# Kernel tuning notes

Hardware: AMD Instinct MI355X
Metric: run time of the kernel (lower is better)

## Reference

```python
import jax, jax.numpy as jnp
import numpy as np

K, D, N, T, B = 8, 16, 32, 200, 2048
_LOG2PI = float(np.log(2.0 * np.pi))


def setup_inputs() -> dict:
    key = jax.random.key(0)
    ks = jax.random.split(key, 13)
    return {
        "discrete_states": jax.random.randint(ks[0], (B, T), 0, K),
        "continuous_states": jax.random.normal(ks[1], (B, T, D), dtype=jnp.float32),
        "obs": jax.random.normal(ks[2], (B, T, N), dtype=jnp.float32),
        "discrete_init_logits": jax.random.normal(ks[3], (K,), dtype=jnp.float32),
        "continuous_init_locs": jax.random.normal(ks[4], (K, D), dtype=jnp.float32),
        "continuous_init_log_scales": jax.random.normal(ks[5], (K, D), dtype=jnp.float32),
        "state_transition_logits": jax.random.normal(ks[6], (K, K), dtype=jnp.float32),
        "dynamics_matrices": jax.random.normal(ks[7], (K, D, D), dtype=jnp.float32) * 0.3,
        "dynamics_offsets": jax.random.normal(ks[8], (K, D), dtype=jnp.float32),
        # NOTE: original code uses dynamics_log_scales directly as a scale (missing .exp());
        # we keep that math faithfully but init it strictly positive to stay finite.
        "dynamics_log_scales": jax.random.uniform(ks[9], (K, D), minval=0.5, maxval=1.5, dtype=jnp.float32),
        "emission_matrices": jax.random.normal(ks[10], (K, N, D), dtype=jnp.float32),
        "emission_offsets": jax.random.normal(ks[11], (K, N), dtype=jnp.float32),
        "emission_log_scales": jax.random.normal(ks[12], (K, N), dtype=jnp.float32),
    }


def _normal_lp(x, loc, scale):
    # elementwise Normal log-prob
    return -0.5 * jnp.square((x - loc) / scale) - jnp.log(scale) - 0.5 * _LOG2PI


def reference(discrete_states, continuous_states, obs,
              discrete_init_logits, continuous_init_locs, continuous_init_log_scales,
              state_transition_logits, dynamics_matrices, dynamics_offsets,
              dynamics_log_scales, emission_matrices, emission_offsets,
              emission_log_scales):
    """log p(s_{1:T}, z_{1:T}, x_{1:T}) -> [B]"""
    s0 = discrete_states[:, 0]                      # [B]
    z0 = continuous_states[:, 0]                    # [B,D]
    # p(s_1)
    lp = jax.nn.log_softmax(discrete_init_logits)[s0]
    # p(z_1 | s_1)
    lp = lp + _normal_lp(z0, continuous_init_locs[s0],
                         jnp.exp(continuous_init_log_scales[s0])).sum(-1)
    # p(s_t | s_{t-1}) for t=2..T, fully vectorized over time
    s_prev = discrete_states[:, :-1]
    s_cur = discrete_states[:, 1:]
    trans = jax.nn.log_softmax(state_transition_logits, axis=-1)  # [K,K]
    lp = lp + trans[s_prev, s_cur].sum(-1)
    # p(z_t | z_{t-1}, s_t)
    A = dynamics_matrices[s_cur]                    # [B,T-1,D,D] gather
    dyn_loc = jnp.einsum('btij,btj->bti', A, continuous_states[:, :-1]) + dynamics_offsets[s_cur]
    dyn_scale = dynamics_log_scales[s_cur]          # faithful: original omits .exp()
    lp = lp + _normal_lp(continuous_states[:, 1:], dyn_loc, dyn_scale).sum((-1, -2))
    # p(x_t | z_t, s_t) for all t
    C = emission_matrices[discrete_states]          # [B,T,N,D] gather
    em_loc = jnp.einsum('btij,btj->bti', C, continuous_states) + emission_offsets[discrete_states]
    em_scale = jnp.exp(emission_log_scales[discrete_states])
    lp = lp + _normal_lp(obs, em_loc, em_scale).sum((-1, -2))
    return lp
```

## Files before the change

kernel.cpp:

```cpp
#include <hip/hip_runtime.h>

#define KK 8
#define DD 16
#define NN 32
#define TT 200
#define BB 2048

#define SCU 260
#define SAU 132
#define SE 36
#define SD 20

#define WS_CU    0
#define WS_AU    2048
#define WS_EMOFF 3072
#define WS_EMINV 3328
#define WS_DYOFF 3584
#define WS_DYINV 3712
#define WS_INLOC 3840
#define WS_ININV 3968
#define WS_TRANS 4096
#define WS_EMC   4160
#define WS_DYC   4168
#define WS_INLP  4176

__device__ __forceinline__ float bflo(unsigned u) { return __uint_as_float(u << 16); }
__device__ __forceinline__ float bfhi(unsigned u) { return __uint_as_float(u & 0xffff0000u); }

__device__ __forceinline__ unsigned bfr(float f) {
  unsigned u = __float_as_uint(f);
  return (u + 0x7fffu + ((u >> 16) & 1u)) >> 16;
}
__device__ __forceinline__ unsigned bfpack(float f0, float f1) {
  return bfr(f0) | (bfr(f1) << 16);
}

__device__ __forceinline__ float dot16bf(const unsigned* __restrict__ row,
                                         const float* __restrict__ z) {
  uint4 w0 = *reinterpret_cast<const uint4*>(row);
  uint4 w1 = *reinterpret_cast<const uint4*>(row + 4);
  float a = bflo(w0.x) * z[0], b = bfhi(w0.x) * z[1];
  a = fmaf(bflo(w0.y), z[2], a);  b = fmaf(bfhi(w0.y), z[3], b);
  a = fmaf(bflo(w0.z), z[4], a);  b = fmaf(bfhi(w0.z), z[5], b);
  a = fmaf(bflo(w0.w), z[6], a);  b = fmaf(bfhi(w0.w), z[7], b);
  a = fmaf(bflo(w1.x), z[8], a);  b = fmaf(bfhi(w1.x), z[9], b);
  a = fmaf(bflo(w1.y), z[10], a); b = fmaf(bfhi(w1.y), z[11], b);
  a = fmaf(bflo(w1.z), z[12], a); b = fmaf(bfhi(w1.z), z[13], b);
  a = fmaf(bflo(w1.w), z[14], a); b = fmaf(bfhi(w1.w), z[15], b);
  return a + b;
}

__global__ __launch_bounds__(256) void prep_kernel(
    const float* __restrict__ initlg, const float* __restrict__ initloc,
    const float* __restrict__ initls, const float* __restrict__ transg,
    const float* __restrict__ Ag, const float* __restrict__ dynoff,
    const float* __restrict__ dynls, const float* __restrict__ Cg,
    const float* __restrict__ emoff, const float* __restrict__ emls,
    unsigned* __restrict__ ws, float* __restrict__ out) {
  const float HALF_LOG2PI = 0.91893853320467274178f;
  const int tid = threadIdx.x;
  float* wsf = reinterpret_cast<float*>(ws);

  for (int i = tid; i < 2048; i += 256)
    ws[WS_CU + i] = bfpack(Cg[2 * i], Cg[2 * i + 1]);
  for (int i = tid; i < 1024; i += 256)
    ws[WS_AU + i] = bfpack(Ag[2 * i], Ag[2 * i + 1]);
  if (tid < 256) { wsf[WS_EMOFF + tid] = emoff[tid]; wsf[WS_EMINV + tid] = expf(-emls[tid]); }
  if (tid < 128) {
    wsf[WS_DYOFF + tid] = dynoff[tid];
    wsf[WS_DYINV + tid] = 1.0f / dynls[tid];
    wsf[WS_INLOC + tid] = initloc[tid];
    wsf[WS_ININV + tid] = expf(-initls[tid]);
  }
  if (tid < 64) {
    int kr = tid >> 3;
    float mx = transg[kr * KK];
    for (int j = 1; j < KK; ++j) mx = fmaxf(mx, transg[kr * KK + j]);
    float ss = 0.f;
    for (int j = 0; j < KK; ++j) ss += expf(transg[kr * KK + j] - mx);
    wsf[WS_TRANS + tid] = transg[tid] - (logf(ss) + mx);
  }
  if (tid < 8) {
    int k = tid;
    float se = 0.f;
    for (int n = 0; n < NN; ++n) se -= emls[k * NN + n];
    wsf[WS_EMC + k] = se - NN * HALF_LOG2PI;
    float sd = 0.f;
    for (int d = 0; d < DD; ++d) sd -= logf(dynls[k * DD + d]);
    wsf[WS_DYC + k] = sd - DD * HALF_LOG2PI;
    float mx = initlg[0];
    for (int j = 1; j < KK; ++j) mx = fmaxf(mx, initlg[j]);
    float ss = 0.f;
    for (int j = 0; j < KK; ++j) ss += expf(initlg[j] - mx);
    float si = 0.f;
    for (int d = 0; d < DD; ++d) si -= initls[k * DD + d];
    wsf[WS_INLP + k] = initlg[k] - (logf(ss) + mx) + si - DD * HALF_LOG2PI;
  }
  for (int i = tid; i < BB; i += 256) out[i] = 0.f;
}

__global__ __launch_bounds__(256) void slds_lp_kernel(
    const int* __restrict__ dsts,
    const float* __restrict__ zg,
    const float* __restrict__ obsg,
    const unsigned* __restrict__ ws,
    float* __restrict__ out)
{
  __shared__ __align__(16) unsigned sCu[KK * SCU];
  __shared__ __align__(16) unsigned sAu[KK * SAU];
  __shared__ __align__(16) float sEmOff[KK * SE];
  __shared__ __align__(16) float sEmInv[KK * SE];
  __shared__ __align__(16) float sDynOff[KK * SD];
  __shared__ __align__(16) float sDynInv[KK * SD];
  __shared__ __align__(16) float sInitLoc[KK * SD];
  __shared__ __align__(16) float sInitInv[KK * SD];
  __shared__ float sTrans[KK * KK];
  __shared__ float sEmConst[KK];
  __shared__ float sDynConst[KK];
  __shared__ float sInitLp[KK];

  const int tid = threadIdx.x;
  const float* wsf = reinterpret_cast<const float*>(ws);

  for (int i = tid; i < 2048; i += 256) {
    int k = i >> 8, r = i & 255;
    sCu[k * SCU + r] = ws[WS_CU + i];
  }
  for (int i = tid; i < 1024; i += 256) {
    int k = i >> 7, r = i & 127;
    sAu[k * SAU + r] = ws[WS_AU + i];
  }
  if (tid < 256) {
    int k = tid >> 5, n = tid & 31;
    sEmOff[k * SE + n] = wsf[WS_EMOFF + tid];
    sEmInv[k * SE + n] = wsf[WS_EMINV + tid];
  }
  if (tid < 128) {
    int k = tid >> 4, d = tid & 15;
    sDynOff[k * SD + d] = wsf[WS_DYOFF + tid];
    sDynInv[k * SD + d] = wsf[WS_DYINV + tid];
    sInitLoc[k * SD + d] = wsf[WS_INLOC + tid];
    sInitInv[k * SD + d] = wsf[WS_ININV + tid];
  }
  if (tid < 64) sTrans[tid] = wsf[WS_TRANS + tid];
  if (tid < 8) {
    sEmConst[tid] = wsf[WS_EMC + tid];
    sDynConst[tid] = wsf[WS_DYC + tid];
    sInitLp[tid] = wsf[WS_INLP + tid];
  }
  __syncthreads();

  const int nItems = BB * TT;
  const int gstride = gridDim.x * blockDim.x;
  for (int item = blockIdx.x * blockDim.x + tid; item < nItems; item += gstride) {
    const int b = item / TT;
    const int t = item - b * TT;
    const int lane = tid & 63;

    float zz[16];
    {
      const float4* p = reinterpret_cast<const float4*>(zg + (size_t)item * DD);
      float4 a0 = p[0], a1 = p[1], a2 = p[2], a3 = p[3];
      zz[0] = a0.x; zz[1] = a0.y; zz[2] = a0.z; zz[3] = a0.w;
      zz[4] = a1.x; zz[5] = a1.y; zz[6] = a1.z; zz[7] = a1.w;
      zz[8] = a2.x; zz[9] = a2.y; zz[10] = a2.z; zz[11] = a2.w;
      zz[12] = a3.x; zz[13] = a3.y; zz[14] = a3.z; zz[15] = a3.w;
    }
    const int s = dsts[item];

    float zpg[4];
    float zp[16];
    int sp = __shfl_up(s, 1, 64);
    if (lane == 0 && t != 0) {
      sp = dsts[item - 1];
      const float4* p = reinterpret_cast<const float4*>(zg + (size_t)(item - 1) * DD);
      float4 a0 = p[0], a1 = p[1], a2 = p[2], a3 = p[3];
      zp[0] = a0.x; zp[1] = a0.y; zp[2] = a0.z; zp[3] = a0.w;
      zp[4] = a1.x; zp[5] = a1.y; zp[6] = a1.z; zp[7] = a1.w;
      zp[8] = a2.x; zp[9] = a2.y; zp[10] = a2.z; zp[11] = a2.w;
      zp[12] = a3.x; zp[13] = a3.y; zp[14] = a3.z; zp[15] = a3.w;
    }
#pragma unroll
    for (int i = 0; i < 16; ++i) {
      float sh = __shfl_up(zz[i], 1, 64);
      if (lane != 0) zp[i] = sh;
    }
    (void)zpg;

    const float4* o4 = reinterpret_cast<const float4*>(obsg + (size_t)item * NN);
    const int cb = s * SCU;
    const int eb4 = s * (SE / 4);
    float acc = 0.f;
#pragma unroll 2
    for (int g = 0; g < 8; ++g) {
      float4 o = o4[g];
      float4 off = reinterpret_cast<const float4*>(sEmOff)[eb4 + g];
      float4 inv = reinterpret_cast<const float4*>(sEmInv)[eb4 + g];
      int n0 = g * 4;
      float l0 = dot16bf(&sCu[cb + (n0 + 0) * 8], zz) + off.x;
      float l1 = dot16bf(&sCu[cb + (n0 + 1) * 8], zz) + off.y;
      float l2 = dot16bf(&sCu[cb + (n0 + 2) * 8], zz) + off.z;
      float l3 = dot16bf(&sCu[cb + (n0 + 3) * 8], zz) + off.w;
      float d0 = (o.x - l0) * inv.x;
      float d1 = (o.y - l1) * inv.y;
      float d2 = (o.z - l2) * inv.z;
      float d3 = (o.w - l3) * inv.w;
      acc = fmaf(d0, d0, acc); acc = fmaf(d1, d1, acc);
      acc = fmaf(d2, d2, acc); acc = fmaf(d3, d3, acc);
    }
    float lp = -0.5f * acc + sEmConst[s];

    if (t != 0) {
      const int ab = s * SAU;
      const int db4 = s * (SD / 4);
      float a2acc = 0.f;
#pragma unroll 2
      for (int g = 0; g < 4; ++g) {
        float4 off = reinterpret_cast<const float4*>(sDynOff)[db4 + g];
        float4 inv = reinterpret_cast<const float4*>(sDynInv)[db4 + g];
        int i0 = g * 4;
        float l0 = dot16bf(&sAu[ab + (i0 + 0) * 8], zp) + off.x;
        float l1 = dot16bf(&sAu[ab + (i0 + 1) * 8], zp) + off.y;
        float l2 = dot16bf(&sAu[ab + (i0 + 2) * 8], zp) + off.z;
        float l3 = dot16bf(&sAu[ab + (i0 + 3) * 8], zp) + off.w;
        float d0 = (zz[i0 + 0] - l0) * inv.x;
        float d1 = (zz[i0 + 1] - l1) * inv.y;
        float d2 = (zz[i0 + 2] - l2) * inv.z;
        float d3 = (zz[i0 + 3] - l3) * inv.w;
        a2acc = fmaf(d0, d0, a2acc); a2acc = fmaf(d1, d1, a2acc);
        a2acc = fmaf(d2, d2, a2acc); a2acc = fmaf(d3, d3, a2acc);
      }
      lp += -0.5f * a2acc + sDynConst[s] + sTrans[sp * KK + s];
    } else {
      const int ib4 = s * (SD / 4);
      float a2acc = 0.f;
#pragma unroll 2
      for (int g = 0; g < 4; ++g) {
        float4 loc = reinterpret_cast<const float4*>(sInitLoc)[ib4 + g];
        float4 inv = reinterpret_cast<const float4*>(sInitInv)[ib4 + g];
        int i0 = g * 4;
        float d0 = (zz[i0 + 0] - loc.x) * inv.x;
        float d1 = (zz[i0 + 1] - loc.y) * inv.y;
        float d2 = (zz[i0 + 2] - loc.z) * inv.z;
        float d3 = (zz[i0 + 3] - loc.w) * inv.w;
        a2acc = fmaf(d0, d0, a2acc); a2acc = fmaf(d1, d1, a2acc);
        a2acc = fmaf(d2, d2, a2acc); a2acc = fmaf(d3, d3, a2acc);
      }
      lp += -0.5f * a2acc + sInitLp[s];
    }

    float v = lp;
#pragma unroll
    for (int off = 1; off < 64; off <<= 1) {
      float ov = __shfl_up(v, off, 64);
      int obk = __shfl_up(b, off, 64);
      if (lane >= off && obk == b) v += ov;
    }
    int nb = __shfl_down(b, 1, 64);
    if (lane == 63 || nb != b) atomicAdd(&out[b], v);
  }
}

extern "C" void kernel_launch(void* const* d_in, const int* in_sizes, int n_in,
                              void* d_out, int out_size, void* d_ws, size_t ws_size,
                              hipStream_t stream) {
  const int*   dsts    = (const int*)d_in[0];
  const float* zg      = (const float*)d_in[1];
  const float* obsg    = (const float*)d_in[2];
  const float* initlg  = (const float*)d_in[3];
  const float* initloc = (const float*)d_in[4];
  const float* initls  = (const float*)d_in[5];
  const float* transg  = (const float*)d_in[6];
  const float* Ag      = (const float*)d_in[7];
  const float* dynoff  = (const float*)d_in[8];
  const float* dynls   = (const float*)d_in[9];
  const float* Cg      = (const float*)d_in[10];
  const float* emoff   = (const float*)d_in[11];
  const float* emls    = (const float*)d_in[12];
  float* out = (float*)d_out;
  unsigned* ws = (unsigned*)d_ws;

  prep_kernel<<<1, 256, 0, stream>>>(initlg, initloc, initls, transg, Ag,
                                     dynoff, dynls, Cg, emoff, emls, ws, out);
  slds_lp_kernel<<<1600, 256, 0, stream>>>(dsts, zg, obsg, ws, out);
}
```

Measured before the change: 144.8 us.

## Use bf16 dot2 instructions with packed z, prefetch obs, simplify segmented scan

Packs the continuous state into bf16 pairs and computes the emission and dynamics dot products with the hardware fdot2 bf16 builtin, roughly halving ALU work per dot product. The previous state is now shuffled as 8 packed words instead of 16 floats. Observation loads are software-prefetched one pair ahead in a non-unrolled loop. The segmented wave reduction uses t instead of shuffling b, which drops several shuffles. Rounding z to bf16 adds precision loss beyond the bf16 weights, and the scan assumes items in a wave are contiguous in t within a batch row.

```diff
diff --git a/kernel.cpp b/kernel.cpp
--- a/kernel.cpp
+++ b/kernel.cpp
@@ -24,6 +24,8 @@
 #define WS_DYC   4168
 #define WS_INLP  4176
 
+typedef __bf16 bf16x2 __attribute__((ext_vector_type(2)));
+
 __device__ __forceinline__ float bflo(unsigned u) { return __uint_as_float(u << 16); }
 __device__ __forceinline__ float bfhi(unsigned u) { return __uint_as_float(u & 0xffff0000u); }
 
@@ -35,18 +37,28 @@
   return bfr(f0) | (bfr(f1) << 16);
 }
 
-__device__ __forceinline__ float dot16bf(const unsigned* __restrict__ row,
-                                         const float* __restrict__ z) {
+__device__ __forceinline__ float dot2bf(unsigned a, unsigned b, float c) {
+#if __has_builtin(__builtin_amdgcn_fdot2_bf16_bf16_f32)
+  return __builtin_amdgcn_fdot2_bf16_bf16_f32(
+      __builtin_bit_cast(bf16x2, a), __builtin_bit_cast(bf16x2, b), c);
+#else
+  float r = fmaf(bflo(a), bflo(b), c);
+  return fmaf(bfhi(a), bfhi(b), r);
+#endif
+}
+
+__device__ __forceinline__ float dot16d2(const unsigned* __restrict__ row,
+                                         const unsigned* __restrict__ zp) {
   uint4 w0 = *reinterpret_cast<const uint4*>(row);
   uint4 w1 = *reinterpret_cast<const uint4*>(row + 4);
-  float a = bflo(w0.x) * z[0], b = bfhi(w0.x) * z[1];
-  a = fmaf(bflo(w0.y), z[2], a);  b = fmaf(bfhi(w0.y), z[3], b);
-  a = fmaf(bflo(w0.z), z[4], a);  b = fmaf(bfhi(w0.z), z[5], b);
-  a = fmaf(bflo(w0.w), z[6], a);  b = fmaf(bfhi(w0.w), z[7], b);
-  a = fmaf(bflo(w1.x), z[8], a);  b = fmaf(bfhi(w1.x), z[9], b);
-  a = fmaf(bflo(w1.y), z[10], a); b = fmaf(bfhi(w1.y), z[11], b);
-  a = fmaf(bflo(w1.z), z[12], a); b = fmaf(bfhi(w1.z), z[13], b);
-  a = fmaf(bflo(w1.w), z[14], a); b = fmaf(bfhi(w1.w), z[15], b);
+  float a = dot2bf(w0.x, zp[0], 0.f);
+  float b = dot2bf(w0.y, zp[1], 0.f);
+  a = dot2bf(w0.z, zp[2], a);
+  b = dot2bf(w0.w, zp[3], b);
+  a = dot2bf(w1.x, zp[4], a);
+  b = dot2bf(w1.y, zp[5], b);
+  a = dot2bf(w1.z, zp[6], a);
+  b = dot2bf(w1.w, zp[7], b);
   return a + b;
 }
 
@@ -158,6 +170,7 @@
     const int lane = tid & 63;
 
     float zz[16];
+    unsigned zzp[8];
     {
       const float4* p = reinterpret_cast<const float4*>(zg + (size_t)item * DD);
       float4 a0 = p[0], a1 = p[1], a2 = p[2], a3 = p[3];
@@ -165,48 +178,53 @@
       zz[4] = a1.x; zz[5] = a1.y; zz[6] = a1.z; zz[7] = a1.w;
       zz[8] = a2.x; zz[9] = a2.y; zz[10] = a2.z; zz[11] = a2.w;
       zz[12] = a3.x; zz[13] = a3.y; zz[14] = a3.z; zz[15] = a3.w;
+#pragma unroll
+      for (int i = 0; i < 8; ++i) zzp[i] = bfpack(zz[2 * i], zz[2 * i + 1]);
     }
     const int s = dsts[item];
 
-    float zpg[4];
-    float zp[16];
+    unsigned zpp[8];
     int sp = __shfl_up(s, 1, 64);
+#pragma unroll
+    for (int i = 0; i < 8; ++i) zpp[i] = __shfl_up(zzp[i], 1, 64);
     if (lane == 0 && t != 0) {
       sp = dsts[item - 1];
       const float4* p = reinterpret_cast<const float4*>(zg + (size_t)(item - 1) * DD);
       float4 a0 = p[0], a1 = p[1], a2 = p[2], a3 = p[3];
-      zp[0] = a0.x; zp[1] = a0.y; zp[2] = a0.z; zp[3] = a0.w;
-      zp[4] = a1.x; zp[5] = a1.y; zp[6] = a1.z; zp[7] = a1.w;
-      zp[8] = a2.x; zp[9] = a2.y; zp[10] = a2.z; zp[11] = a2.w;
-      zp[12] = a3.x; zp[13] = a3.y; zp[14] = a3.z; zp[15] = a3.w;
-    }
-#pragma unroll
-    for (int i = 0; i < 16; ++i) {
-      float sh = __shfl_up(zz[i], 1, 64);
-      if (lane != 0) zp[i] = sh;
-    }
-    (void)zpg;
+      zpp[0] = bfpack(a0.x, a0.y); zpp[1] = bfpack(a0.z, a0.w);
+      zpp[2] = bfpack(a1.x, a1.y); zpp[3] = bfpack(a1.z, a1.w);
+      zpp[4] = bfpack(a2.x, a2.y); zpp[5] = bfpack(a2.z, a2.w);
+      zpp[6] = bfpack(a3.x, a3.y); zpp[7] = bfpack(a3.z, a3.w);
+    }
 
     const float4* o4 = reinterpret_cast<const float4*>(obsg + (size_t)item * NN);
     const int cb = s * SCU;
     const int eb4 = s * (SE / 4);
+    float4 oa = o4[0], ob = o4[1];
     float acc = 0.f;
-#pragma unroll 2
-    for (int g = 0; g < 8; ++g) {
-      float4 o = o4[g];
-      float4 off = reinterpret_cast<const float4*>(sEmOff)[eb4 + g];
-      float4 inv = reinterpret_cast<const float4*>(sEmInv)[eb4 + g];
-      int n0 = g * 4;
-      float l0 = dot16bf(&sCu[cb + (n0 + 0) * 8], zz) + off.x;
-      float l1 = dot16bf(&sCu[cb + (n0 + 1) * 8], zz) + off.y;
-      float l2 = dot16bf(&sCu[cb + (n0 + 2) * 8], zz) + off.z;
-      float l3 = dot16bf(&sCu[cb + (n0 + 3) * 8], zz) + off.w;
-      float d0 = (o.x - l0) * inv.x;
-      float d1 = (o.y - l1) * inv.y;
-      float d2 = (o.z - l2) * inv.z;
-      float d3 = (o.w - l3) * inv.w;
-      acc = fmaf(d0, d0, acc); acc = fmaf(d1, d1, acc);
-      acc = fmaf(d2, d2, acc); acc = fmaf(d3, d3, acc);
+#pragma unroll 1
+    for (int gg = 0; gg < 4; ++gg) {
+      float4 na = oa, nb = ob;
+      if (gg < 3) { na = o4[2 * gg + 2]; nb = o4[2 * gg + 3]; }
+#pragma unroll
+      for (int h = 0; h < 2; ++h) {
+        const int g = 2 * gg + h;
+        float4 o = h ? ob : oa;
+        float4 off = reinterpret_cast<const float4*>(sEmOff)[eb4 + g];
+        float4 inv = reinterpret_cast<const float4*>(sEmInv)[eb4 + g];
+        int n0 = g * 4;
+        float l0 = dot16d2(&sCu[cb + (n0 + 0) * 8], zzp) + off.x;
+        float l1 = dot16d2(&sCu[cb + (n0 + 1) * 8], zzp) + off.y;
+        float l2 = dot16d2(&sCu[cb + (n0 + 2) * 8], zzp) + off.z;
+        float l3 = dot16d2(&sCu[cb + (n0 + 3) * 8], zzp) + off.w;
+        float d0 = (o.x - l0) * inv.x;
+        float d1 = (o.y - l1) * inv.y;
+        float d2 = (o.z - l2) * inv.z;
+        float d3 = (o.w - l3) * inv.w;
+        acc = fmaf(d0, d0, acc); acc = fmaf(d1, d1, acc);
+        acc = fmaf(d2, d2, acc); acc = fmaf(d3, d3, acc);
+      }
+      oa = na; ob = nb;
     }
     float lp = -0.5f * acc + sEmConst[s];
 
@@ -219,10 +237,10 @@
         float4 off = reinterpret_cast<const float4*>(sDynOff)[db4 + g];
         float4 inv = reinterpret_cast<const float4*>(sDynInv)[db4 + g];
         int i0 = g * 4;
-        float l0 = dot16bf(&sAu[ab + (i0 + 0) * 8], zp) + off.x;
-        float l1 = dot16bf(&sAu[ab + (i0 + 1) * 8], zp) + off.y;
-        float l2 = dot16bf(&sAu[ab + (i0 + 2) * 8], zp) + off.z;
-        float l3 = dot16bf(&sAu[ab + (i0 + 3) * 8], zp) + off.w;
+        float l0 = dot16d2(&sAu[ab + (i0 + 0) * 8], zpp) + off.x;
+        float l1 = dot16d2(&sAu[ab + (i0 + 1) * 8], zpp) + off.y;
+        float l2 = dot16d2(&sAu[ab + (i0 + 2) * 8], zpp) + off.z;
+        float l3 = dot16d2(&sAu[ab + (i0 + 3) * 8], zpp) + off.w;
         float d0 = (zz[i0 + 0] - l0) * inv.x;
         float d1 = (zz[i0 + 1] - l1) * inv.y;
         float d2 = (zz[i0 + 2] - l2) * inv.z;
@@ -253,11 +271,9 @@
 #pragma unroll
     for (int off = 1; off < 64; off <<= 1) {
       float ov = __shfl_up(v, off, 64);
-      int obk = __shfl_up(b, off, 64);
-      if (lane >= off && obk == b) v += ov;
-    }
-    int nb = __shfl_down(b, 1, 64);
-    if (lane == 63 || nb != b) atomicAdd(&out[b], v);
+      if (t >= off && lane >= off) v += ov;
+    }
+    if (lane == 63 || t == TT - 1) atomicAdd(&out[b], v);
   }
 }
 
```

New measurement: 146.5 us. Within noise of the previous version (+1.2%).
